# Kernel tuning notes

Measured on AMD Instinct MI355X. Metric: run time of the kernel, lower is better.

Reference implementation:

```python
import jax, jax.numpy as jnp
import numpy as np

N_NODES = 100000
N_EDGES = 1600000
D_FEAT = 48
N_LAYERS = 3  # GCN(n_layers=3) builds exactly 3 GraphConv layers


def setup_inputs() -> dict:
    key = jax.random.key(0)
    k1, k2, k3 = jax.random.split(key, 3)
    features = jax.random.normal(k1, (N_NODES, D_FEAT), dtype=jnp.float32)
    src = jax.random.randint(k2, (N_EDGES,), 0, N_NODES, dtype=jnp.int32)
    dst = jax.random.randint(k3, (N_EDGES,), 0, N_NODES, dtype=jnp.int32)
    return {"features": features, "src": src, "dst": dst}


def reference(features, src, dst):
    # GraphConv(norm='none', weight=False, bias=False): h_v = sum_{u->v} h_u, then activation.
    # Layers 0..N_LAYERS-2 apply relu; the final layer has no activation.
    h = features
    for i in range(N_LAYERS):
        msgs = h[src]  # gather source features per edge: [E, D]
        h = jax.ops.segment_sum(msgs, dst, num_segments=N_NODES)  # scatter-add to dst
        if i < N_LAYERS - 1:
            h = jax.nn.relu(h)
    return h
```

## Files before the change

kernel.cpp:

```cpp
#include <hip/hip_runtime.h>

#define D 48
#define BSH 8
#define BN 256
#define NBMAX 400
#define CH 256
#define CAPT 5120

static __device__ inline unsigned int f2bf_rne(float x) {
    unsigned int u = __float_as_uint(x);
    return (u + 0x7FFFu + ((u >> 16) & 1u)) >> 16;
}
static __device__ inline unsigned int pack2(float lo, float hi) {
    return f2bf_rne(lo) | (f2bf_rne(hi) << 16);
}
static __device__ inline float bf_lo(unsigned int u) { return __uint_as_float(u << 16); }
static __device__ inline float bf_hi(unsigned int u) { return __uint_as_float(u & 0xFFFF0000u); }


__global__ void k_front(const int* __restrict__ dst, const float* __restrict__ feat,
                        uint2* __restrict__ featb, int* __restrict__ btot,
                        int* __restrict__ cbase, int E, int NB, int CHE, int N) {
    int t = threadIdx.x;
    if (blockIdx.x < CH) {
        int c = blockIdx.x;
        __shared__ int h[NBMAX];
        for (int b = t; b < NB; b += 1024) h[b] = 0;
        __syncthreads();
        int lo = c * CHE, hi = min(lo + CHE, E);
        for (int i = lo + t; i < hi; i += 1024)
            atomicAdd(&h[dst[i] >> BSH], 1);
        __syncthreads();
        for (int b = t; b < NB; b += 1024)
            cbase[c * NB + b] = atomicAdd(&btot[b], h[b]);
    } else {
        const float4* f4 = (const float4*)feat;
        int total = N * 16;
        int i = (blockIdx.x - CH) * 1024 + t;
        int stride = 256 * 1024;
        for (; i < total; i += stride) {
            int node = i >> 4, c = i & 15;
            uint2 v = make_uint2(0u, 0u);
            if (c < 12) {
                float4 f = f4[node * 12 + c];
                v = make_uint2(pack2(f.x, f.y), pack2(f.z, f.w));
            }
            featb[i] = v;
        }
    }
}


__global__ void k_bscan(const int* __restrict__ btot, int* __restrict__ bbase,
                        int* __restrict__ row_ptr, int NB, int N, int E) {
    __shared__ int sh[256];
    __shared__ int srun;
    int t = threadIdx.x;
    if (t == 0) srun = 0;
    __syncthreads();
    int nch = (NB + 255) / 256;
    for (int c = 0; c < nch; c++) {
        int b = c * 256 + t;
        int v = (b < NB) ? btot[b] : 0;
        sh[t] = v;
        __syncthreads();
        for (int off = 1; off < 256; off <<= 1) {
            int u = (t >= off) ? sh[t - off] : 0;
            __syncthreads();
            sh[t] += u;
            __syncthreads();
        }
        int run = srun;
        if (b < NB) bbase[b] = run + sh[t] - v;
        __syncthreads();
        if (t == 255) srun = run + sh[255];
        __syncthreads();
    }
    if (t == 0) { bbase[NB] = E; row_ptr[N] = E; }
}


__global__ void k_scatter(const int* __restrict__ src, const int* __restrict__ dst,
                          const int* __restrict__ bbase, const int* __restrict__ cbase,
                          int* __restrict__ stage, int E, int NB, int CHE) {
    int c = blockIdx.x;
    int t = threadIdx.x;
    __shared__ int cur[NBMAX];
    for (int b = t; b < NB; b += blockDim.x)
        cur[b] = bbase[b] + cbase[c * NB + b];
    __syncthreads();
    int lo = c * CHE, hi = min(lo + CHE, E);
    for (int i = lo + t; i < hi; i += blockDim.x) {
        int s = src[i], d = dst[i];
        int p = atomicAdd(&cur[d >> BSH], 1);
        stage[p] = ((d & (BN - 1)) << 17) | s;
    }
}


__global__ void k_build(const int* __restrict__ stage, const int* __restrict__ bbase,
                        int* __restrict__ row_ptr, int* __restrict__ esrc,
                        int N, int NB) {
    int b = blockIdx.x;
    int t = threadIdx.x;
    __shared__ int lbuf[CAPT];
    __shared__ int lout[CAPT];
    __shared__ int hist[BN];
    __shared__ int cur[BN];
    __shared__ int sh[BN];
    int base = bbase[b];
    int cnt = min(bbase[b + 1] - base, CAPT);
    hist[t] = 0;
    __syncthreads();
    for (int i = t; i < cnt; i += 256) {
        int v = stage[base + i];
        lbuf[i] = v;
        atomicAdd(&hist[v >> 17], 1);
    }
    __syncthreads();
    int orig = hist[t];
    sh[t] = orig;
    __syncthreads();
    for (int off = 1; off < 256; off <<= 1) {
        int u = (t >= off) ? sh[t - off] : 0;
        __syncthreads();
        sh[t] += u;
        __syncthreads();
    }
    int excl = sh[t] - orig;
    cur[t] = excl;
    int node = (b << BSH) + t;
    if (node < N) row_ptr[node] = base + excl;
    __syncthreads();
    for (int i = t; i < cnt; i += 256) {
        int v = lbuf[i];
        int p = atomicAdd(&cur[v >> 17], 1);
        lout[p] = v & 0x1FFFF;
    }
    __syncthreads();
    for (int i = t; i < cnt; i += 256) esrc[base + i] = lout[i];
}


template <int RELU, int OUTF32>
__global__ void k_pull(const uint4* __restrict__ hin, void* __restrict__ hout,
                       const int* __restrict__ row_ptr, const int* __restrict__ esrc,
                       int n) {
    int grp = threadIdx.x >> 4;
    int lane = threadIdx.x & 15;
    int side = lane >> 3;
    int sub = lane & 7;
    int node = blockIdx.x * 16 + grp;
    if (node >= n) return;
    int jb = row_ptr[node], je = row_ptr[node + 1];
    float a0 = 0.f, a1 = 0.f, a2 = 0.f, a3 = 0.f, a4 = 0.f, a5 = 0.f, a6 = 0.f, a7 = 0.f;
    int j = jb;
    for (; j + 8 <= je; j += 8) {
        int s0 = esrc[j + 0 + side];
        int s1 = esrc[j + 2 + side];
        int s2 = esrc[j + 4 + side];
        int s3 = esrc[j + 6 + side];
        uint4 q0 = hin[s0 * 8 + sub];
        uint4 q1 = hin[s1 * 8 + sub];
        uint4 q2 = hin[s2 * 8 + sub];
        uint4 q3 = hin[s3 * 8 + sub];
        a0 += bf_lo(q0.x); a1 += bf_hi(q0.x); a2 += bf_lo(q0.y); a3 += bf_hi(q0.y);
        a4 += bf_lo(q0.z); a5 += bf_hi(q0.z); a6 += bf_lo(q0.w); a7 += bf_hi(q0.w);
        a0 += bf_lo(q1.x); a1 += bf_hi(q1.x); a2 += bf_lo(q1.y); a3 += bf_hi(q1.y);
        a4 += bf_lo(q1.z); a5 += bf_hi(q1.z); a6 += bf_lo(q1.w); a7 += bf_hi(q1.w);
        a0 += bf_lo(q2.x); a1 += bf_hi(q2.x); a2 += bf_lo(q2.y); a3 += bf_hi(q2.y);
        a4 += bf_lo(q2.z); a5 += bf_hi(q2.z); a6 += bf_lo(q2.w); a7 += bf_hi(q2.w);
        a0 += bf_lo(q3.x); a1 += bf_hi(q3.x); a2 += bf_lo(q3.y); a3 += bf_hi(q3.y);
        a4 += bf_lo(q3.z); a5 += bf_hi(q3.z); a6 += bf_lo(q3.w); a7 += bf_hi(q3.w);
    }
    for (; j + 2 <= je; j += 2) {
        int s0 = esrc[j + side];
        uint4 q0 = hin[s0 * 8 + sub];
        a0 += bf_lo(q0.x); a1 += bf_hi(q0.x); a2 += bf_lo(q0.y); a3 += bf_hi(q0.y);
        a4 += bf_lo(q0.z); a5 += bf_hi(q0.z); a6 += bf_lo(q0.w); a7 += bf_hi(q0.w);
    }
    if (j < je && side == 0) {
        int s0 = esrc[j];
        uint4 q0 = hin[s0 * 8 + sub];
        a0 += bf_lo(q0.x); a1 += bf_hi(q0.x); a2 += bf_lo(q0.y); a3 += bf_hi(q0.y);
        a4 += bf_lo(q0.z); a5 += bf_hi(q0.z); a6 += bf_lo(q0.w); a7 += bf_hi(q0.w);
    }
    a0 += __shfl_xor(a0, 8); a1 += __shfl_xor(a1, 8);
    a2 += __shfl_xor(a2, 8); a3 += __shfl_xor(a3, 8);
    a4 += __shfl_xor(a4, 8); a5 += __shfl_xor(a5, 8);
    a6 += __shfl_xor(a6, 8); a7 += __shfl_xor(a7, 8);
    if (RELU) {
        a0 = fmaxf(a0, 0.f); a1 = fmaxf(a1, 0.f); a2 = fmaxf(a2, 0.f); a3 = fmaxf(a3, 0.f);
        a4 = fmaxf(a4, 0.f); a5 = fmaxf(a5, 0.f); a6 = fmaxf(a6, 0.f); a7 = fmaxf(a7, 0.f);
    }
    if (side != 0) return;
    if (OUTF32) {
        if (sub < 6) {
            float* o = (float*)hout + (size_t)node * D + 8 * sub;
            *(float4*)(o)     = make_float4(a0, a1, a2, a3);
            *(float4*)(o + 4) = make_float4(a4, a5, a6, a7);
        }
    } else {
        uint4* o = (uint4*)hout + node * 8 + sub;
        *o = make_uint4(pack2(a0, a1), pack2(a2, a3), pack2(a4, a5), pack2(a6, a7));
    }
}

extern "C" void kernel_launch(void* const* d_in, const int* in_sizes, int n_in,
                              void* d_out, int out_size, void* d_ws, size_t ws_size,
                              hipStream_t stream) {
    const float* feat = (const float*)d_in[0];
    const int* src = (const int*)d_in[1];
    const int* dst = (const int*)d_in[2];
    int N = in_sizes[0] / D;
    int E = in_sizes[1];
    int NB = (N + BN - 1) >> BSH;
    int CHE = (E + CH - 1) / CH;

    char* ws = (char*)d_ws;
    int*   btot    = (int*)(ws + ((size_t)0 << 10));
    int*   bbase   = (int*)(ws + ((size_t)64 << 10));
    int*   cbase   = (int*)(ws + ((size_t)128 << 10));
    int*   row_ptr = (int*)(ws + ((size_t)640 << 10));
    int*   esrc    = (int*)(ws + ((size_t)2 << 20));
    uint2* featb   = (uint2*)(ws + ((size_t)9 << 20));
    int*   stage   = (int*)(ws + ((size_t)22 << 20));
    uint4* hb0     = (uint4*)(ws + ((size_t)22 << 20));

    hipMemsetAsync(btot, 0, (size_t)NB * sizeof(int), stream);

    k_front<<<CH + 256, 1024, 0, stream>>>(dst, feat, featb, btot, cbase, E, NB, CHE, N);
    k_bscan<<<1, 256, 0, stream>>>(btot, bbase, row_ptr, NB, N, E);
    k_scatter<<<CH, 1024, 0, stream>>>(src, dst, bbase, cbase, stage, E, NB, CHE);
    k_build<<<NB, 256, 0, stream>>>(stage, bbase, row_ptr, esrc, N, NB);

    int pg = (N + 15) / 16;
    k_pull<1, 0><<<pg, 256, 0, stream>>>((const uint4*)featb, hb0, row_ptr, esrc, N);
    k_pull<1, 0><<<pg, 256, 0, stream>>>((const uint4*)hb0, featb, row_ptr, esrc, N);
    k_pull<0, 1><<<pg, 256, 0, stream>>>((const uint4*)featb, d_out, row_ptr, esrc, N);
}
```

Baseline: 205.0 us.

## Split bf16 feature table into three column slabs for cache-friendly gathers

Feature storage changes from 64-byte padded rows (48 bf16 + padding) to three separate 16-column slabs, each 32 bytes per node. Each pull kernel now processes one slab per block group, with block index selecting the slab, so each pass gathers from a 3.2MB table that fits better in cache. It also drops the padding bytes from gather traffic. In exchange, row_ptr and esrc are read three times per layer and the gathers are narrower (uint2 per lane).

```diff
diff --git a/kernel.cpp b/kernel.cpp
--- a/kernel.cpp
+++ b/kernel.cpp
@@ -35,17 +35,14 @@
             cbase[c * NB + b] = atomicAdd(&btot[b], h[b]);
     } else {
         const float4* f4 = (const float4*)feat;
-        int total = N * 16;
+        int total = N * 12;
         int i = (blockIdx.x - CH) * 1024 + t;
         int stride = 256 * 1024;
         for (; i < total; i += stride) {
-            int node = i >> 4, c = i & 15;
-            uint2 v = make_uint2(0u, 0u);
-            if (c < 12) {
-                float4 f = f4[node * 12 + c];
-                v = make_uint2(pack2(f.x, f.y), pack2(f.z, f.w));
-            }
-            featb[i] = v;
+            int n = i / 12, k = i - n * 12;
+            float4 f = f4[i];
+            int p = k >> 2, s = k & 3;
+            featb[((size_t)p * N + n) * 4 + s] = make_uint2(pack2(f.x, f.y), pack2(f.z, f.w));
         }
     }
 }
@@ -143,66 +140,57 @@
 
 
 template <int RELU, int OUTF32>
-__global__ void k_pull(const uint4* __restrict__ hin, void* __restrict__ hout,
-                       const int* __restrict__ row_ptr, const int* __restrict__ esrc,
-                       int n) {
-    int grp = threadIdx.x >> 4;
-    int lane = threadIdx.x & 15;
-    int side = lane >> 3;
-    int sub = lane & 7;
-    int node = blockIdx.x * 16 + grp;
+__global__ void k_pull3(const uint2* __restrict__ hin, void* __restrict__ hout,
+                        const int* __restrict__ row_ptr, const int* __restrict__ esrc,
+                        int n, int pgp) {
+    int pass = blockIdx.x / pgp;
+    int nb = blockIdx.x - pass * pgp;
+    int grp = threadIdx.x >> 3;
+    int side = (threadIdx.x >> 2) & 1;
+    int sub = threadIdx.x & 3;
+    int node = nb * 32 + grp;
     if (node >= n) return;
+    const uint2* tab = hin + ((size_t)pass * n) * 4;
     int jb = row_ptr[node], je = row_ptr[node + 1];
-    float a0 = 0.f, a1 = 0.f, a2 = 0.f, a3 = 0.f, a4 = 0.f, a5 = 0.f, a6 = 0.f, a7 = 0.f;
+    float a0 = 0.f, a1 = 0.f, a2 = 0.f, a3 = 0.f;
     int j = jb;
     for (; j + 8 <= je; j += 8) {
         int s0 = esrc[j + 0 + side];
         int s1 = esrc[j + 2 + side];
         int s2 = esrc[j + 4 + side];
         int s3 = esrc[j + 6 + side];
-        uint4 q0 = hin[s0 * 8 + sub];
-        uint4 q1 = hin[s1 * 8 + sub];
-        uint4 q2 = hin[s2 * 8 + sub];
-        uint4 q3 = hin[s3 * 8 + sub];
+        uint2 q0 = tab[s0 * 4 + sub];
+        uint2 q1 = tab[s1 * 4 + sub];
+        uint2 q2 = tab[s2 * 4 + sub];
+        uint2 q3 = tab[s3 * 4 + sub];
         a0 += bf_lo(q0.x); a1 += bf_hi(q0.x); a2 += bf_lo(q0.y); a3 += bf_hi(q0.y);
-        a4 += bf_lo(q0.z); a5 += bf_hi(q0.z); a6 += bf_lo(q0.w); a7 += bf_hi(q0.w);
         a0 += bf_lo(q1.x); a1 += bf_hi(q1.x); a2 += bf_lo(q1.y); a3 += bf_hi(q1.y);
-        a4 += bf_lo(q1.z); a5 += bf_hi(q1.z); a6 += bf_lo(q1.w); a7 += bf_hi(q1.w);
         a0 += bf_lo(q2.x); a1 += bf_hi(q2.x); a2 += bf_lo(q2.y); a3 += bf_hi(q2.y);
-        a4 += bf_lo(q2.z); a5 += bf_hi(q2.z); a6 += bf_lo(q2.w); a7 += bf_hi(q2.w);
         a0 += bf_lo(q3.x); a1 += bf_hi(q3.x); a2 += bf_lo(q3.y); a3 += bf_hi(q3.y);
-        a4 += bf_lo(q3.z); a5 += bf_hi(q3.z); a6 += bf_lo(q3.w); a7 += bf_hi(q3.w);
     }
     for (; j + 2 <= je; j += 2) {
         int s0 = esrc[j + side];
-        uint4 q0 = hin[s0 * 8 + sub];
+        uint2 q0 = tab[s0 * 4 + sub];
         a0 += bf_lo(q0.x); a1 += bf_hi(q0.x); a2 += bf_lo(q0.y); a3 += bf_hi(q0.y);
-        a4 += bf_lo(q0.z); a5 += bf_hi(q0.z); a6 += bf_lo(q0.w); a7 += bf_hi(q0.w);
     }
     if (j < je && side == 0) {
         int s0 = esrc[j];
-        uint4 q0 = hin[s0 * 8 + sub];
+        uint2 q0 = tab[s0 * 4 + sub];
         a0 += bf_lo(q0.x); a1 += bf_hi(q0.x); a2 += bf_lo(q0.y); a3 += bf_hi(q0.y);
-        a4 += bf_lo(q0.z); a5 += bf_hi(q0.z); a6 += bf_lo(q0.w); a7 += bf_hi(q0.w);
-    }
-    a0 += __shfl_xor(a0, 8); a1 += __shfl_xor(a1, 8);
-    a2 += __shfl_xor(a2, 8); a3 += __shfl_xor(a3, 8);
-    a4 += __shfl_xor(a4, 8); a5 += __shfl_xor(a5, 8);
-    a6 += __shfl_xor(a6, 8); a7 += __shfl_xor(a7, 8);
+    }
+    a0 += __shfl_xor(a0, 4); a1 += __shfl_xor(a1, 4);
+    a2 += __shfl_xor(a2, 4); a3 += __shfl_xor(a3, 4);
     if (RELU) {
-        a0 = fmaxf(a0, 0.f); a1 = fmaxf(a1, 0.f); a2 = fmaxf(a2, 0.f); a3 = fmaxf(a3, 0.f);
-        a4 = fmaxf(a4, 0.f); a5 = fmaxf(a5, 0.f); a6 = fmaxf(a6, 0.f); a7 = fmaxf(a7, 0.f);
+        a0 = fmaxf(a0, 0.f); a1 = fmaxf(a1, 0.f);
+        a2 = fmaxf(a2, 0.f); a3 = fmaxf(a3, 0.f);
     }
     if (side != 0) return;
     if (OUTF32) {
-        if (sub < 6) {
-            float* o = (float*)hout + (size_t)node * D + 8 * sub;
-            *(float4*)(o)     = make_float4(a0, a1, a2, a3);
-            *(float4*)(o + 4) = make_float4(a4, a5, a6, a7);
-        }
+        float* o = (float*)hout + (size_t)node * D + pass * 16 + sub * 4;
+        *(float4*)o = make_float4(a0, a1, a2, a3);
     } else {
-        uint4* o = (uint4*)hout + node * 8 + sub;
-        *o = make_uint4(pack2(a0, a1), pack2(a2, a3), pack2(a4, a5), pack2(a6, a7));
+        uint2* o = (uint2*)hout + ((size_t)pass * n + node) * 4 + sub;
+        *o = make_uint2(pack2(a0, a1), pack2(a2, a3));
     }
 }
 
@@ -224,8 +212,8 @@
     int*   row_ptr = (int*)(ws + ((size_t)640 << 10));
     int*   esrc    = (int*)(ws + ((size_t)2 << 20));
     uint2* featb   = (uint2*)(ws + ((size_t)9 << 20));
-    int*   stage   = (int*)(ws + ((size_t)22 << 20));
-    uint4* hb0     = (uint4*)(ws + ((size_t)22 << 20));
+    int*   stage   = (int*)(ws + ((size_t)19 << 20));
+    uint2* hb0     = (uint2*)(ws + ((size_t)26 << 20));
 
     hipMemsetAsync(btot, 0, (size_t)NB * sizeof(int), stream);
 
@@ -234,8 +222,9 @@
     k_scatter<<<CH, 1024, 0, stream>>>(src, dst, bbase, cbase, stage, E, NB, CHE);
     k_build<<<NB, 256, 0, stream>>>(stage, bbase, row_ptr, esrc, N, NB);
 
-    int pg = (N + 15) / 16;
-    k_pull<1, 0><<<pg, 256, 0, stream>>>((const uint4*)featb, hb0, row_ptr, esrc, N);
-    k_pull<1, 0><<<pg, 256, 0, stream>>>((const uint4*)hb0, featb, row_ptr, esrc, N);
-    k_pull<0, 1><<<pg, 256, 0, stream>>>((const uint4*)featb, d_out, row_ptr, esrc, N);
-}
+    int pgp = (N + 31) / 32;
+    int pg = 3 * pgp;
+    k_pull3<1, 0><<<pg, 256, 0, stream>>>(featb, hb0, row_ptr, esrc, N, pgp);
+    k_pull3<1, 0><<<pg, 256, 0, stream>>>(hb0, featb, row_ptr, esrc, N, pgp);
+    k_pull3<0, 1><<<pg, 256, 0, stream>>>(featb, d_out, row_ptr, esrc, N, pgp);
+}
```

Measured after the change: 228.2 us. +11.3%, slower.

## Fuse bucket scan into scatter kernel and deepen pull gather unroll

Applied to the files above, without the earlier changes.

Drops the single-block bucket-prefix-scan kernel. Each scatter block now redundantly scans the bucket totals in shared memory with 1024 threads, and block 0 writes bbase and row_ptr[N]. This removes one kernel launch and a serial scan stage. Separately, the pull kernel's main loop now handles 16 edges per iteration with 8 outstanding gathers per lane instead of 4, which raises memory-level parallelism at the cost of more registers and a longer remainder loop for low-degree nodes.

```diff
diff --git a/kernel.cpp b/kernel.cpp
--- a/kernel.cpp
+++ b/kernel.cpp
@@ -51,46 +51,32 @@
 }
 
 
-__global__ void k_bscan(const int* __restrict__ btot, int* __restrict__ bbase,
-                        int* __restrict__ row_ptr, int NB, int N, int E) {
-    __shared__ int sh[256];
-    __shared__ int srun;
-    int t = threadIdx.x;
-    if (t == 0) srun = 0;
-    __syncthreads();
-    int nch = (NB + 255) / 256;
-    for (int c = 0; c < nch; c++) {
-        int b = c * 256 + t;
-        int v = (b < NB) ? btot[b] : 0;
-        sh[t] = v;
-        __syncthreads();
-        for (int off = 1; off < 256; off <<= 1) {
-            int u = (t >= off) ? sh[t - off] : 0;
-            __syncthreads();
-            sh[t] += u;
-            __syncthreads();
-        }
-        int run = srun;
-        if (b < NB) bbase[b] = run + sh[t] - v;
-        __syncthreads();
-        if (t == 255) srun = run + sh[255];
-        __syncthreads();
-    }
-    if (t == 0) { bbase[NB] = E; row_ptr[N] = E; }
-}
-
-
 __global__ void k_scatter(const int* __restrict__ src, const int* __restrict__ dst,
-                          const int* __restrict__ bbase, const int* __restrict__ cbase,
-                          int* __restrict__ stage, int E, int NB, int CHE) {
+                          const int* __restrict__ btot, const int* __restrict__ cbase,
+                          int* __restrict__ stage, int* __restrict__ bbase,
+                          int* __restrict__ row_ptr, int E, int NB, int CHE, int N) {
     int c = blockIdx.x;
     int t = threadIdx.x;
+    __shared__ int sh[1024];
     __shared__ int cur[NBMAX];
-    for (int b = t; b < NB; b += blockDim.x)
-        cur[b] = bbase[b] + cbase[c * NB + b];
+    int v = (t < NB) ? btot[t] : 0;
+    sh[t] = v;
+    __syncthreads();
+    for (int off = 1; off < 1024; off <<= 1) {
+        int u = (t >= off) ? sh[t - off] : 0;
+        __syncthreads();
+        sh[t] += u;
+        __syncthreads();
+    }
+    int excl = sh[t] - v;
+    if (t < NB) cur[t] = excl + cbase[c * NB + t];
+    if (c == 0) {
+        if (t < NB) bbase[t] = excl;
+        if (t == NB) { bbase[NB] = excl; row_ptr[N] = excl; }
+    }
     __syncthreads();
     int lo = c * CHE, hi = min(lo + CHE, E);
-    for (int i = lo + t; i < hi; i += blockDim.x) {
+    for (int i = lo + t; i < hi; i += 1024) {
         int s = src[i], d = dst[i];
         int p = atomicAdd(&cur[d >> BSH], 1);
         stage[p] = ((d & (BN - 1)) << 17) | s;
@@ -155,23 +141,18 @@
     int jb = row_ptr[node], je = row_ptr[node + 1];
     float a0 = 0.f, a1 = 0.f, a2 = 0.f, a3 = 0.f, a4 = 0.f, a5 = 0.f, a6 = 0.f, a7 = 0.f;
     int j = jb;
-    for (; j + 8 <= je; j += 8) {
-        int s0 = esrc[j + 0 + side];
-        int s1 = esrc[j + 2 + side];
-        int s2 = esrc[j + 4 + side];
-        int s3 = esrc[j + 6 + side];
-        uint4 q0 = hin[s0 * 8 + sub];
-        uint4 q1 = hin[s1 * 8 + sub];
-        uint4 q2 = hin[s2 * 8 + sub];
-        uint4 q3 = hin[s3 * 8 + sub];
-        a0 += bf_lo(q0.x); a1 += bf_hi(q0.x); a2 += bf_lo(q0.y); a3 += bf_hi(q0.y);
-        a4 += bf_lo(q0.z); a5 += bf_hi(q0.z); a6 += bf_lo(q0.w); a7 += bf_hi(q0.w);
-        a0 += bf_lo(q1.x); a1 += bf_hi(q1.x); a2 += bf_lo(q1.y); a3 += bf_hi(q1.y);
-        a4 += bf_lo(q1.z); a5 += bf_hi(q1.z); a6 += bf_lo(q1.w); a7 += bf_hi(q1.w);
-        a0 += bf_lo(q2.x); a1 += bf_hi(q2.x); a2 += bf_lo(q2.y); a3 += bf_hi(q2.y);
-        a4 += bf_lo(q2.z); a5 += bf_hi(q2.z); a6 += bf_lo(q2.w); a7 += bf_hi(q2.w);
-        a0 += bf_lo(q3.x); a1 += bf_hi(q3.x); a2 += bf_lo(q3.y); a3 += bf_hi(q3.y);
-        a4 += bf_lo(q3.z); a5 += bf_hi(q3.z); a6 += bf_lo(q3.w); a7 += bf_hi(q3.w);
+    for (; j + 16 <= je; j += 16) {
+        int s[8];
+#pragma unroll
+        for (int u = 0; u < 8; u++) s[u] = esrc[j + 2 * u + side];
+        uint4 q[8];
+#pragma unroll
+        for (int u = 0; u < 8; u++) q[u] = hin[s[u] * 8 + sub];
+#pragma unroll
+        for (int u = 0; u < 8; u++) {
+            a0 += bf_lo(q[u].x); a1 += bf_hi(q[u].x); a2 += bf_lo(q[u].y); a3 += bf_hi(q[u].y);
+            a4 += bf_lo(q[u].z); a5 += bf_hi(q[u].z); a6 += bf_lo(q[u].w); a7 += bf_hi(q[u].w);
+        }
     }
     for (; j + 2 <= je; j += 2) {
         int s0 = esrc[j + side];
@@ -230,8 +211,7 @@
     hipMemsetAsync(btot, 0, (size_t)NB * sizeof(int), stream);
 
     k_front<<<CH + 256, 1024, 0, stream>>>(dst, feat, featb, btot, cbase, E, NB, CHE, N);
-    k_bscan<<<1, 256, 0, stream>>>(btot, bbase, row_ptr, NB, N, E);
-    k_scatter<<<CH, 1024, 0, stream>>>(src, dst, bbase, cbase, stage, E, NB, CHE);
+    k_scatter<<<CH, 1024, 0, stream>>>(src, dst, btot, cbase, stage, bbase, row_ptr, E, NB, CHE, N);
     k_build<<<NB, 256, 0, stream>>>(stage, bbase, row_ptr, esrc, N, NB);
 
     int pg = (N + 15) / 16;
```

Measured after the change: 226.4 us. 10.5% more time.
